# Optimization experiments

Measured on AMD Instinct MI355X. Metric: run time of the kernel, lower is better.

The kernel has to match this reference:

```python
import jax, jax.numpy as jnp
import numpy as np

B, C, L, H = 4, 128, 4096, 4
GROUPS, EPS = 32, 1e-5


def group_norm(x, gamma, beta):
    # x: [B, C, L]; normalize per (batch, group) over (C//G, L)
    b, c, l = x.shape
    xg = x.reshape(b, GROUPS, c // GROUPS, l)
    mu = jnp.mean(xg, axis=(2, 3), keepdims=True)
    var = jnp.var(xg, axis=(2, 3), keepdims=True)
    xn = ((xg - mu) * jax.lax.rsqrt(var + EPS)).reshape(b, c, l)
    return xn * gamma[None, :, None] + beta[None, :, None]


def setup_inputs() -> dict:
    key = jax.random.key(0)
    k1, k2, k3 = jax.random.split(key, 3)
    return {
        "x": jax.random.normal(k1, (B, C, L), dtype=jnp.float32),
        "w_qkv": jax.random.normal(k2, (3 * C, C), dtype=jnp.float32) * 0.02,
        "w_proj": jax.random.normal(k3, (C, C), dtype=jnp.float32) * 0.02,
        "b_proj": jnp.zeros((C,), dtype=jnp.float32),
        "gn_gamma": jnp.ones((C,), dtype=jnp.float32),
        "gn_beta": jnp.zeros((C,), dtype=jnp.float32),
    }


def reference(x, w_qkv, w_proj, b_proj, gn_gamma, gn_beta):
    b, c, l = x.shape
    hd = c // H
    h = group_norm(x, gn_gamma, gn_beta)
    # 1x1 conv == channel matmul: [B, 3C, L]
    qkv = jnp.einsum('oc,bcl->bol', w_qkv, h)
    # torch reshape(B*H, 3C/H, L).chunk(3, dim=1): per-head contiguous slices
    qkv = qkv.reshape(b, H, 3 * hd, l)
    q, k, v = qkv[:, :, :hd], qkv[:, :, hd:2 * hd], qkv[:, :, 2 * hd:]
    scale = 1.0 / np.sqrt(np.sqrt(hd)).astype(np.float32)
    attn = jnp.einsum('bhct,bhcs->bhts', q * scale, k * scale)
    attn = jax.nn.softmax(attn, axis=-1)
    o = jnp.einsum('bhts,bhcs->bhct', attn, v).reshape(b, c, l)
    o = jnp.einsum('oc,bcl->bol', w_proj, o) + b_proj[None, :, None]
    return o + x
```

## Files before the change

kernel.cpp:

```cpp
#include <hip/hip_runtime.h>
#include <hip/hip_bf16.h>
#include <cstdint>
#include <cstddef>


#define B_ 4
#define C_ 128
#define L_ 4096
#define H_ 4
#define HD_ 32
#define NG_ 32
#define CPG_ 4
#define EPS_ 1e-5f
#define QKSCALE_ 0.5050097650430367f

typedef __attribute__((ext_vector_type(8))) short bf16x8;
typedef __attribute__((ext_vector_type(8))) unsigned short u16x8;
typedef __attribute__((ext_vector_type(4))) float f32x4;
typedef __attribute__((ext_vector_type(2))) _Float16 f16x2;
typedef __attribute__((ext_vector_type(4))) _Float16 f16x4;

#if __has_builtin(__builtin_amdgcn_exp2f)
#define EXP2F(x) __builtin_amdgcn_exp2f(x)
#else
#define EXP2F(x) exp2f(x)
#endif

#define MFMA_PV(a, b, c) __builtin_amdgcn_mfma_f32_16x16x16f16((a), (b), (c), 0, 0, 0)

__device__ __forceinline__ float bu2f(unsigned short u) {
  return __builtin_bit_cast(float, (unsigned int)(((unsigned int)u) << 16));
}
__device__ __forceinline__ unsigned short f2bu(float f) {
  unsigned int u = __builtin_bit_cast(unsigned int, f);
  unsigned int r = (u + 0x7fffu + ((u >> 16) & 1u)) >> 16;
  return (unsigned short)r;
}
__device__ __forceinline__ float4 u42f4(ushort4 u) {
  return make_float4(bu2f(u.x), bu2f(u.y), bu2f(u.z), bu2f(u.w));
}
__device__ __forceinline__ unsigned int pkbf(float a, float b) {
  return (unsigned int)f2bu(a) | ((unsigned int)f2bu(b) << 16);
}
__device__ __forceinline__ f16x2 pkhf2(float a, float b) {
#if __has_builtin(__builtin_amdgcn_cvt_pkrtz)
  return __builtin_bit_cast(f16x2, __builtin_amdgcn_cvt_pkrtz(a, b));
#else
  f16x2 r;
  r[0] = (_Float16)a;
  r[1] = (_Float16)b;
  return r;
#endif
}
__device__ __forceinline__ unsigned int pkhf(float a, float b) {
  return __builtin_bit_cast(unsigned int, pkhf2(a, b));
}

__device__ __forceinline__ bool detect_fast(const ushort* x) {
  __shared__ int flag_s;
  int t = threadIdx.x;
  if (t < 64) {
    int e = (x[t] >> 7) & 0xFF;
    unsigned long long m = __ballot((e < 64) || (e > 192));
    if (t == 0) flag_s = (__popcll(m) > 4) ? 1 : 0;
  }
  __syncthreads();
  return flag_s != 0;
}

__device__ __forceinline__ float4 ldx4(const void* x, size_t idx, bool f32) {
  if (f32) return *((const float4*)x + (idx >> 2));
  ushort4 u = *((const ushort4*)x + (idx >> 2));
  return u42f4(u);
}

__global__ __launch_bounds__(256) void gn_stats(const void* __restrict__ x,
                                                const void* __restrict__ wq,
                                                const void* __restrict__ wp,
                                                const void* __restrict__ bp,
                                                const void* __restrict__ gm,
                                                const void* __restrict__ bt,
                                                ushort* __restrict__ wq_b,
                                                ushort* __restrict__ wp_b,
                                                float* __restrict__ bp_f,
                                                float2* __restrict__ gn_ab) {
  bool f32 = detect_fast((const ushort*)x);
  int blk = blockIdx.x;
  int t = threadIdx.x;

  if (blk >= 128) {
    int i0 = ((blk - 128) * 256 + t) * 8;
#pragma unroll
    for (int k = 0; k < 8; ++k) {
      int i = i0 + k;
      if (i >= 65664) break;
      if (i < 49152) {
        wq_b[i] = f32 ? f2bu(((const float*)wq)[i]) : ((const ushort*)wq)[i];
      } else if (i < 65536) {
        int off = i - 49152;
        wp_b[off] = f32 ? f2bu(((const float*)wp)[off]) : ((const ushort*)wp)[off];
      } else {
        int off = i - 65536;
        bp_f[off] = f32 ? ((const float*)bp)[off] : bu2f(((const ushort*)bp)[off]);
      }
    }
    return;
  }

  int b = blk >> 5, g = blk & 31;
  size_t base = ((size_t)b * C_ + (size_t)g * CPG_) * L_;

  float s = 0.f, ss = 0.f;
#pragma unroll
  for (int i = 0; i < 16; ++i) {
    size_t e = base + i * 1024 + t * 4;
    float4 f = ldx4(x, e, f32);
    s += f.x + f.y + f.z + f.w;
    ss += f.x * f.x + f.y * f.y + f.z * f.z + f.w * f.w;
  }
#pragma unroll
  for (int m = 32; m >= 1; m >>= 1) {
    s += __shfl_xor(s, m, 64);
    ss += __shfl_xor(ss, m, 64);
  }
  __shared__ float red[4][2];
  int wv = t >> 6;
  if ((t & 63) == 0) { red[wv][0] = s; red[wv][1] = ss; }
  __syncthreads();
  float ts = red[0][0] + red[1][0] + red[2][0] + red[3][0];
  float tss = red[0][1] + red[1][1] + red[2][1] + red[3][1];
  float mu = ts * (1.0f / 16384.0f);
  float var = tss * (1.0f / 16384.0f) - mu * mu;
  float rs = rsqrtf(var + EPS_);

  if (t < CPG_) {
    int gi = g * CPG_ + t;
    float ga = f32 ? ((const float*)gm)[gi] : bu2f(((const ushort*)gm)[gi]);
    float be = f32 ? ((const float*)bt)[gi] : bu2f(((const ushort*)bt)[gi]);
    gn_ab[b * C_ + gi] = make_float2(ga * rs, be - mu * ga * rs);
  }
}

__global__ __launch_bounds__(256) void qkv_kernel(const ushort* __restrict__ wq_b,
                                                  const void* __restrict__ x,
                                                  const float2* __restrict__ gn_ab,
                                                  ushort* __restrict__ Qt,
                                                  ushort* __restrict__ Kt,
                                                  ushort* __restrict__ Vb) {
  bool f32 = detect_fast((const ushort*)x);
  __shared__ alignas(16) ushort Hs[64][136];
  __shared__ alignas(16) float Ls[64][69];

  int lx = blockIdx.x, oz = blockIdx.y, b = blockIdx.z;
  int t = threadIdx.x;
  int w = t >> 6, lane = t & 63, l16 = lane & 15, q = lane >> 4, q8 = q * 8;

  {
    int u = t & 63, lh = (t >> 6) * 16;
    int c0 = 2 * u;
    float2 ab0 = gn_ab[b * C_ + c0];
    float2 ab1 = gn_ab[b * C_ + c0 + 1];
    size_t xo = ((size_t)b * C_ + c0) * L_ + (size_t)lx * 64 + lh;
#pragma unroll
    for (int j = 0; j < 4; ++j) {
      float4 f0 = ldx4(x, xo + j * 4, f32);
      float4 f1 = ldx4(x, xo + L_ + j * 4, f32);
      float n0[4] = {f0.x * ab0.x + ab0.y, f0.y * ab0.x + ab0.y,
                     f0.z * ab0.x + ab0.y, f0.w * ab0.x + ab0.y};
      float n1[4] = {f1.x * ab1.x + ab1.y, f1.y * ab1.x + ab1.y,
                     f1.z * ab1.x + ab1.y, f1.w * ab1.x + ab1.y};
#pragma unroll
      for (int k = 0; k < 4; ++k)
        *(unsigned int*)&Hs[lh + j * 4 + k][c0] = pkbf(n0[k], n1[k]);
    }
  }
  __syncthreads();

  for (int j = 0; j < 2; ++j) {
    int oy = oz * 2 + j;
    const ushort* wg = wq_b + (size_t)(oy * 64 + w * 16 + l16) * C_;

    f32x4 acc[4] = {{0.f, 0.f, 0.f, 0.f}, {0.f, 0.f, 0.f, 0.f},
                    {0.f, 0.f, 0.f, 0.f}, {0.f, 0.f, 0.f, 0.f}};
#pragma unroll
    for (int kc = 0; kc < 4; ++kc) {
      bf16x8 aw = *(const bf16x8*)(wg + kc * 32 + q8);
#pragma unroll
      for (int nb = 0; nb < 4; ++nb) {
        bf16x8 bh = *(const bf16x8*)&Hs[nb * 16 + l16][kc * 32 + q8];
        acc[nb] = __builtin_amdgcn_mfma_f32_16x16x32_bf16(aw, bh, acc[nb], 0, 0, 0);
      }
    }
    __syncthreads();
#pragma unroll
    for (int nb = 0; nb < 4; ++nb)
#pragma unroll
      for (int r = 0; r < 4; ++r)
        Ls[nb * 16 + l16][w * 16 + 4 * q + r] = acc[nb][r];
    __syncthreads();

#pragma unroll
    for (int hhalf = 0; hhalf < 2; ++hhalf) {
      int hh = oy * 2 + hhalf;
      int type = hh % 3, head = hh / 3;
      size_t bh = (size_t)b * H_ + head;
      if (type == 2) {
        int c_loc = t >> 3, l8 = (t & 7) * 8;
        float v[8];
#pragma unroll
        for (int jj = 0; jj < 8; ++jj) v[jj] = Ls[l8 + jj][hhalf * 32 + c_loc];
        uint4 u;
        u.x = pkhf(v[0], v[1]);
        u.y = pkhf(v[2], v[3]);
        u.z = pkhf(v[4], v[5]);
        u.w = pkhf(v[6], v[7]);
        *(uint4*)(Vb + (bh * 32 + c_loc) * L_ + (size_t)lx * 64 + l8) = u;
      } else {
        ushort* dst = type ? Kt : Qt;
        int l = t >> 2, seg = (t & 3) * 8;
        const float* src = &Ls[l][hhalf * 32 + seg];
        uint4 u;
        u.x = pkbf(src[0] * QKSCALE_, src[1] * QKSCALE_);
        u.y = pkbf(src[2] * QKSCALE_, src[3] * QKSCALE_);
        u.z = pkbf(src[4] * QKSCALE_, src[5] * QKSCALE_);
        u.w = pkbf(src[6] * QKSCALE_, src[7] * QKSCALE_);
        *(uint4*)(dst + ((bh * L_) + lx * 64 + l) * 32 + seg) = u;
      }
    }
  }
}

__global__ __launch_bounds__(256) void attn_kernel(const ushort* __restrict__ Qt,
                                                   const ushort* __restrict__ Kt,
                                                   const ushort* __restrict__ Vb,
                                                   ushort* __restrict__ ot) {
  __shared__ alignas(16) ushort Ks[2][4096];
  __shared__ alignas(16) ushort Vs[2][32][136];

  int t = threadIdx.x;
  int w = t >> 6, lane = t & 63, l16 = lane & 15, q = lane >> 4;
  int tq0 = blockIdx.x * 128;
  int bh = blockIdx.y;
  int b = bh >> 2, head = bh & 3;
  const ushort* Qg = Qt + ((size_t)bh * L_ + tq0) * 32;
  const ushort* Kg = Kt + (size_t)bh * L_ * 32;
  const ushort* Vg = Vb + (size_t)bh * 32 * L_;

  int krow = (t & 15) | ((t >> 6) << 4);
  int kq8 = ((t >> 4) & 3) * 8;
  const ushort* kgp = Kg + (size_t)krow * 32 + kq8;
  int vc = t >> 3, vsl = (t & 7) * 8;
  const ushort* vgp = Vg + (size_t)vc * L_ + vsl;
  int trow = w * 16 + l16;
  int q8 = q * 8, q4 = q * 4;

  bf16x8 qfrag0 = *(const bf16x8*)(Qg + (size_t)trow * 32 + q8);
  bf16x8 qfrag1 = *(const bf16x8*)(Qg + (size_t)(64 + trow) * 32 + q8);
  f16x4 ones;
#pragma unroll
  for (int i = 0; i < 4; ++i) ones[i] = (_Float16)1.0f;

  *(uint4*)&Ks[0][t * 8] = *(const uint4*)kgp;
  *(uint4*)&Ks[0][2048 + t * 8] = *(const uint4*)(kgp + 2048);
  *(uint4*)&Vs[0][vc][vsl] = *(const uint4*)vgp;
  *(uint4*)&Vs[0][vc][64 + vsl] = *(const uint4*)(vgp + 64);
  __syncthreads();

  f32x4 aA0 = {0.f, 0.f, 0.f, 0.f}, aB0 = {0.f, 0.f, 0.f, 0.f};
  f32x4 aA1 = {0.f, 0.f, 0.f, 0.f}, aB1 = {0.f, 0.f, 0.f, 0.f};
  f32x4 aL0 = {0.f, 0.f, 0.f, 0.f}, aL1 = {0.f, 0.f, 0.f, 0.f};
  const ushort* kg_n = kgp + 4096;
  const ushort* vg_n = vgp + 128;

#pragma unroll 2
  for (int it = 0; it < 32; ++it) {
    int bc = it & 1;
    if (it < 31) {
      *(uint4*)&Ks[bc ^ 1][t * 8] = *(const uint4*)kg_n;
      *(uint4*)&Ks[bc ^ 1][2048 + t * 8] = *(const uint4*)(kg_n + 2048);
      *(uint4*)&Vs[bc ^ 1][vc][vsl] = *(const uint4*)vg_n;
      *(uint4*)&Vs[bc ^ 1][vc][64 + vsl] = *(const uint4*)(vg_n + 64);
      kg_n += 4096;
      vg_n += 128;
    }

#pragma unroll
    for (int hh2 = 0; hh2 < 2; ++hh2) {
      const ushort* kf = &Ks[bc][hh2 * 2048 + lane * 8];
      bf16x8 ak0 = *(const bf16x8*)(kf);
      bf16x8 ak1 = *(const bf16x8*)(kf + 512);
      bf16x8 ak2 = *(const bf16x8*)(kf + 1024);
      bf16x8 ak3 = *(const bf16x8*)(kf + 1536);
      f32x4 z = {0.f, 0.f, 0.f, 0.f};
      f32x4 sf0[4], sf1[4];
      sf0[0] = __builtin_amdgcn_mfma_f32_16x16x32_bf16(ak0, qfrag0, z, 0, 0, 0);
      sf0[1] = __builtin_amdgcn_mfma_f32_16x16x32_bf16(ak1, qfrag0, z, 0, 0, 0);
      sf0[2] = __builtin_amdgcn_mfma_f32_16x16x32_bf16(ak2, qfrag0, z, 0, 0, 0);
      sf0[3] = __builtin_amdgcn_mfma_f32_16x16x32_bf16(ak3, qfrag0, z, 0, 0, 0);
      sf1[0] = __builtin_amdgcn_mfma_f32_16x16x32_bf16(ak0, qfrag1, z, 0, 0, 0);
      sf1[1] = __builtin_amdgcn_mfma_f32_16x16x32_bf16(ak1, qfrag1, z, 0, 0, 0);
      sf1[2] = __builtin_amdgcn_mfma_f32_16x16x32_bf16(ak2, qfrag1, z, 0, 0, 0);
      sf1[3] = __builtin_amdgcn_mfma_f32_16x16x32_bf16(ak3, qfrag1, z, 0, 0, 0);

#pragma unroll
      for (int n = 0; n < 4; ++n) {
        f16x4 va0 = *(const f16x4*)&Vs[bc][l16][hh2 * 64 + n * 16 + q4];
        f16x4 va1 = *(const f16x4*)&Vs[bc][16 + l16][hh2 * 64 + n * 16 + q4];
        {
          float p0 = EXP2F(sf0[n][0]);
          float p1 = EXP2F(sf0[n][1]);
          float p2 = EXP2F(sf0[n][2]);
          float p3 = EXP2F(sf0[n][3]);
          f16x2 e01 = pkhf2(p0, p1);
          f16x2 e23 = pkhf2(p2, p3);
          f16x4 pb = __builtin_shufflevector(e01, e23, 0, 1, 2, 3);
          aA0 = MFMA_PV(va0, pb, aA0);
          aB0 = MFMA_PV(va1, pb, aB0);
          aL0 = MFMA_PV(ones, pb, aL0);
        }
        {
          float p0 = EXP2F(sf1[n][0]);
          float p1 = EXP2F(sf1[n][1]);
          float p2 = EXP2F(sf1[n][2]);
          float p3 = EXP2F(sf1[n][3]);
          f16x2 e01 = pkhf2(p0, p1);
          f16x2 e23 = pkhf2(p2, p3);
          f16x4 pb = __builtin_shufflevector(e01, e23, 0, 1, 2, 3);
          aA1 = MFMA_PV(va0, pb, aA1);
          aB1 = MFMA_PV(va1, pb, aB1);
          aL1 = MFMA_PV(ones, pb, aL1);
        }
      }
    }
    __syncthreads();
  }

  float inv0 = 1.0f / aL0[0];
  float inv1 = 1.0f / aL1[0];

  __syncthreads();
  ushort* Ep = &Ks[0][0];
#pragma unroll
  for (int r = 0; r < 2; ++r) {
    *(unsigned int*)&Ep[trow * 40 + q4 + 2 * r] =
        pkbf(aA0[2 * r] * inv0, aA0[2 * r + 1] * inv0);
    *(unsigned int*)&Ep[trow * 40 + 16 + q4 + 2 * r] =
        pkbf(aB0[2 * r] * inv0, aB0[2 * r + 1] * inv0);
    *(unsigned int*)&Ep[(64 + trow) * 40 + q4 + 2 * r] =
        pkbf(aA1[2 * r] * inv1, aA1[2 * r + 1] * inv1);
    *(unsigned int*)&Ep[(64 + trow) * 40 + 16 + q4 + 2 * r] =
        pkbf(aB1[2 * r] * inv1, aB1[2 * r + 1] * inv1);
  }
  __syncthreads();
  {
    int row = t >> 2, seg = (t & 3) * 8;
#pragma unroll
    for (int p = 0; p < 2; ++p) {
      *(uint4*)(ot + ((size_t)b * L_ + tq0 + p * 64 + row) * C_ + head * 32 + seg) =
          *(const uint4*)&Ep[(p * 64 + row) * 40 + seg];
    }
  }
}

__global__ __launch_bounds__(256) void proj_kernel(const ushort* __restrict__ wp_b,
                                                   const float* __restrict__ bias,
                                                   const void* __restrict__ x,
                                                   const ushort* __restrict__ ot,
                                                   void* __restrict__ out) {
  bool f32 = detect_fast((const ushort*)x);
  __shared__ alignas(16) float Ls[64][37];

  int lx = blockIdx.x, oy = blockIdx.y, b = blockIdx.z;
  int t = threadIdx.x;
  int w = t >> 6, lane = t & 63, l16 = lane & 15, q = lane >> 4, q8 = q * 8;

  const ushort* wg = wp_b + (size_t)(oy * 64 + w * 16 + l16) * C_;
  const ushort* og = ot + ((size_t)b * L_ + (size_t)lx * 32) * C_;

  f32x4 acc[2] = {{0.f, 0.f, 0.f, 0.f}, {0.f, 0.f, 0.f, 0.f}};
#pragma unroll
  for (int kc = 0; kc < 4; ++kc) {
    bf16x8 aw = *(const bf16x8*)(wg + kc * 32 + q8);
#pragma unroll
    for (int nb = 0; nb < 2; ++nb) {
      bf16x8 bo = *(const bf16x8*)(og + (size_t)(nb * 16 + l16) * C_ + kc * 32 + q8);
      acc[nb] = __builtin_amdgcn_mfma_f32_16x16x32_bf16(aw, bo, acc[nb], 0, 0, 0);
    }
  }
#pragma unroll
  for (int nb = 0; nb < 2; ++nb)
#pragma unroll
    for (int r = 0; r < 4; ++r)
      Ls[w * 16 + 4 * q + r][nb * 16 + l16] = acc[nb][r];
  __syncthreads();

  {
    int o_loc = t >> 2, ls0 = (t & 3) * 8;
    float bv = bias[oy * 64 + o_loc];
    size_t off = ((size_t)b * C_ + oy * 64 + o_loc) * L_ + (size_t)lx * 32 + ls0;
#pragma unroll
    for (int jj = 0; jj < 2; ++jj) {
      float4 xf = ldx4(x, off + jj * 4, f32);
      const float* sp = &Ls[o_loc][ls0 + jj * 4];
      float4 r = make_float4(sp[0] + bv + xf.x, sp[1] + bv + xf.y,
                             sp[2] + bv + xf.z, sp[3] + bv + xf.w);
      if (f32) {
        *(float4*)((float*)out + off + jj * 4) = r;
      } else {
        *(ushort4*)((ushort*)out + off + jj * 4) =
            make_ushort4(f2bu(r.x), f2bu(r.y), f2bu(r.z), f2bu(r.w));
      }
    }
  }
}

extern "C" void kernel_launch(void* const* d_in, const int* in_sizes, int n_in,
                              void* d_out, int out_size, void* d_ws, size_t ws_size,
                              hipStream_t stream) {
  const void* x      = d_in[0];
  const void* w_qkv  = d_in[1];
  const void* w_proj = d_in[2];
  const void* b_proj = d_in[3];
  const void* gamma  = d_in[4];
  const void* beta   = d_in[5];

  char* wsb = (char*)d_ws;
  ushort* wq_b  = (ushort*)(wsb + 0);
  ushort* wp_b  = (ushort*)(wsb + 98304);
  float*  bp_f  = (float*)(wsb + 131072);
  float2* gn_ab = (float2*)(wsb + 131584);
  ushort* Qt    = (ushort*)(wsb + 8388608);
  ushort* Kt    = (ushort*)(wsb + 12582912);
  ushort* Vb    = (ushort*)(wsb + 16777216);
  ushort* ot    = (ushort*)(wsb + 20971520);

  gn_stats<<<dim3(161), dim3(256), 0, stream>>>(x, w_qkv, w_proj, b_proj, gamma, beta,
                                                wq_b, wp_b, bp_f, gn_ab);
  qkv_kernel<<<dim3(L_ / 64, 3, B_), dim3(256), 0, stream>>>(wq_b, x, gn_ab, Qt, Kt, Vb);
  attn_kernel<<<dim3(L_ / 128, B_ * H_), dim3(256), 0, stream>>>(Qt, Kt, Vb, ot);
  proj_kernel<<<dim3(L_ / 32, C_ / 64, B_), dim3(256), 0, stream>>>(wp_b, bp_f, x, ot, d_out);
}
```

Baseline: 149.4 us.

## Split attention key range across two blocks and add combine kernel

Splits each attention block's key/value sweep into two halves along a new grid dimension, writing unnormalized fp32 partial outputs and row sums to workspace. A new combine kernel adds the partials, normalizes, and packs to bf16 for the projection. The original grid was only 32x16=512 blocks, so this doubles parallelism to fill the 256 CUs better. In exchange it adds an extra launch and extra fp32 traffic (about 16MB written and read). It relies on softmax needing no running max, which holds because the scores are bounded.

```diff
diff --git a/kernel.cpp b/kernel.cpp
--- a/kernel.cpp
+++ b/kernel.cpp
@@ -233,7 +233,8 @@
 __global__ __launch_bounds__(256) void attn_kernel(const ushort* __restrict__ Qt,
                                                    const ushort* __restrict__ Kt,
                                                    const ushort* __restrict__ Vb,
-                                                   ushort* __restrict__ ot) {
+                                                   float* __restrict__ op,
+                                                   float* __restrict__ lp) {
   __shared__ alignas(16) ushort Ks[2][4096];
   __shared__ alignas(16) ushort Vs[2][32][136];
 
@@ -241,16 +242,18 @@
   int w = t >> 6, lane = t & 63, l16 = lane & 15, q = lane >> 4;
   int tq0 = blockIdx.x * 128;
   int bh = blockIdx.y;
+  int half = blockIdx.z;
   int b = bh >> 2, head = bh & 3;
   const ushort* Qg = Qt + ((size_t)bh * L_ + tq0) * 32;
   const ushort* Kg = Kt + (size_t)bh * L_ * 32;
   const ushort* Vg = Vb + (size_t)bh * 32 * L_;
 
+  int s0 = half * 2048;
   int krow = (t & 15) | ((t >> 6) << 4);
   int kq8 = ((t >> 4) & 3) * 8;
-  const ushort* kgp = Kg + (size_t)krow * 32 + kq8;
+  const ushort* kgp = Kg + (size_t)(s0 + krow) * 32 + kq8;
   int vc = t >> 3, vsl = (t & 7) * 8;
-  const ushort* vgp = Vg + (size_t)vc * L_ + vsl;
+  const ushort* vgp = Vg + (size_t)vc * L_ + s0 + vsl;
   int trow = w * 16 + l16;
   int q8 = q * 8, q4 = q * 4;
 
@@ -273,9 +276,9 @@
   const ushort* vg_n = vgp + 128;
 
 #pragma unroll 2
-  for (int it = 0; it < 32; ++it) {
+  for (int it = 0; it < 16; ++it) {
     int bc = it & 1;
-    if (it < 31) {
+    if (it < 15) {
       *(uint4*)&Ks[bc ^ 1][t * 8] = *(const uint4*)kg_n;
       *(uint4*)&Ks[bc ^ 1][2048 + t * 8] = *(const uint4*)(kg_n + 2048);
       *(uint4*)&Vs[bc ^ 1][vc][vsl] = *(const uint4*)vg_n;
@@ -335,31 +338,56 @@
     __syncthreads();
   }
 
-  float inv0 = 1.0f / aL0[0];
-  float inv1 = 1.0f / aL1[0];
-
-  __syncthreads();
-  ushort* Ep = &Ks[0][0];
-#pragma unroll
-  for (int r = 0; r < 2; ++r) {
-    *(unsigned int*)&Ep[trow * 40 + q4 + 2 * r] =
-        pkbf(aA0[2 * r] * inv0, aA0[2 * r + 1] * inv0);
-    *(unsigned int*)&Ep[trow * 40 + 16 + q4 + 2 * r] =
-        pkbf(aB0[2 * r] * inv0, aB0[2 * r + 1] * inv0);
-    *(unsigned int*)&Ep[(64 + trow) * 40 + q4 + 2 * r] =
-        pkbf(aA1[2 * r] * inv1, aA1[2 * r + 1] * inv1);
-    *(unsigned int*)&Ep[(64 + trow) * 40 + 16 + q4 + 2 * r] =
-        pkbf(aB1[2 * r] * inv1, aB1[2 * r + 1] * inv1);
-  }
-  __syncthreads();
-  {
-    int row = t >> 2, seg = (t & 3) * 8;
-#pragma unroll
-    for (int p = 0; p < 2; ++p) {
-      *(uint4*)(ot + ((size_t)b * L_ + tq0 + p * 64 + row) * C_ + head * 32 + seg) =
-          *(const uint4*)&Ep[(p * 64 + row) * 40 + seg];
-    }
-  }
+  __syncthreads();
+  float* Ep32 = (float*)&Ks[0][0];
+  size_t opBase = (size_t)half * (B_ * L_ * C_) + ((size_t)b * L_ + tq0) * C_ + head * 32;
+#pragma unroll
+  for (int p = 0; p < 2; ++p) {
+    f32x4 vA = p ? aA1 : aA0;
+    f32x4 vB = p ? aB1 : aB0;
+#pragma unroll
+    for (int r = 0; r < 4; ++r) {
+      Ep32[trow * 40 + q4 + r] = vA[r];
+      Ep32[trow * 40 + 16 + q4 + r] = vB[r];
+    }
+    if (q == 0)
+      lp[((size_t)half * 16 + bh) * L_ + tq0 + p * 64 + trow] = p ? aL1[0] : aL0[0];
+    __syncthreads();
+    {
+      int row = t >> 2, seg = (t & 3) * 8;
+      float* dst = op + opBase + (size_t)(p * 64 + row) * C_ + seg;
+      *(float4*)dst = *(const float4*)&Ep32[row * 40 + seg];
+      *(float4*)(dst + 4) = *(const float4*)&Ep32[row * 40 + seg + 4];
+    }
+    __syncthreads();
+  }
+}
+
+__global__ __launch_bounds__(256) void combine_kernel(const float* __restrict__ op,
+                                                      const float* __restrict__ lp,
+                                                      ushort* __restrict__ ot) {
+  int idx = blockIdx.x * 256 + threadIdx.x;
+  int e0 = idx * 8;
+  int c0 = e0 & 127;
+  int l = (e0 >> 7) & (L_ - 1);
+  int b = e0 >> 19;
+  int head = c0 >> 5;
+  int bh = b * H_ + head;
+  float l1 = lp[(size_t)bh * L_ + l];
+  float l2 = lp[(size_t)(16 + bh) * L_ + l];
+  float inv = 1.0f / (l1 + l2);
+  const float* p0 = op + (size_t)e0;
+  const float* p1 = op + (size_t)(B_ * L_ * C_) + e0;
+  float4 a0 = *(const float4*)p0;
+  float4 a1 = *(const float4*)(p0 + 4);
+  float4 b0 = *(const float4*)p1;
+  float4 b1 = *(const float4*)(p1 + 4);
+  uint4 u;
+  u.x = pkbf((a0.x + b0.x) * inv, (a0.y + b0.y) * inv);
+  u.y = pkbf((a0.z + b0.z) * inv, (a0.w + b0.w) * inv);
+  u.z = pkbf((a1.x + b1.x) * inv, (a1.y + b1.y) * inv);
+  u.w = pkbf((a1.z + b1.z) * inv, (a1.w + b1.w) * inv);
+  *(uint4*)(ot + e0) = u;
 }
 
 __global__ __launch_bounds__(256) void proj_kernel(const ushort* __restrict__ wp_b,
@@ -429,14 +457,17 @@
   ushort* wp_b  = (ushort*)(wsb + 98304);
   float*  bp_f  = (float*)(wsb + 131072);
   float2* gn_ab = (float2*)(wsb + 131584);
+  float*  lp    = (float*)(wsb + 1048576);
   ushort* Qt    = (ushort*)(wsb + 8388608);
   ushort* Kt    = (ushort*)(wsb + 12582912);
   ushort* Vb    = (ushort*)(wsb + 16777216);
   ushort* ot    = (ushort*)(wsb + 20971520);
+  float*  op    = (float*)(wsb + 25165824);
 
   gn_stats<<<dim3(161), dim3(256), 0, stream>>>(x, w_qkv, w_proj, b_proj, gamma, beta,
                                                 wq_b, wp_b, bp_f, gn_ab);
   qkv_kernel<<<dim3(L_ / 64, 3, B_), dim3(256), 0, stream>>>(wq_b, x, gn_ab, Qt, Kt, Vb);
-  attn_kernel<<<dim3(L_ / 128, B_ * H_), dim3(256), 0, stream>>>(Qt, Kt, Vb, ot);
+  attn_kernel<<<dim3(L_ / 128, B_ * H_, 2), dim3(256), 0, stream>>>(Qt, Kt, Vb, op, lp);
+  combine_kernel<<<dim3(2097152 / (256 * 8)), dim3(256), 0, stream>>>(op, lp, ot);
   proj_kernel<<<dim3(L_ / 32, C_ / 64, B_), dim3(256), 0, stream>>>(wp_b, bp_f, x, ot, d_out);
 }
```

Result: no change. 149.7 us (+0.2%).
